# Kernel tuning notes

Measured on AMD Instinct MI355X. Metric: run time of the kernel, lower is better.

## Reference

```python
import jax, jax.numpy as jnp
import numpy as np

B, T, F, H = 8192, 96, 64, 256


def setup_inputs() -> dict:
    key = jax.random.key(0)
    ks = jax.random.split(key, 8)
    s = 0.05
    return {
        "decoder_feature": jax.random.normal(ks[0], (B, T, F), jnp.float32),
        "init_state": jax.random.normal(ks[1], (B, H), jnp.float32),
        "decoder_init_input": jax.random.normal(ks[2], (B, 1), jnp.float32),
        "kernel": jax.random.normal(ks[3], (1 + F, 3 * H), jnp.float32) * s,
        "recurrent_kernel": jax.random.normal(ks[4], (H, 3 * H), jnp.float32) * s,
        "input_bias": jnp.zeros((3 * H,), jnp.float32),
        "recurrent_bias": jnp.zeros((3 * H,), jnp.float32),
        "dense_w": jax.random.normal(ks[5], (H, 1), jnp.float32) * s,
        "dense_b": jnp.zeros((1,), jnp.float32),
        "predict_seq_length": T,
    }


def reference(decoder_feature, init_state, decoder_init_input, kernel,
              recurrent_kernel, input_bias, recurrent_bias, dense_w, dense_b,
              predict_seq_length):
    # teacher=None, use_attention=False path of Decoder2.forward.
    # Keras GRUCell (reset_after=True) recurrence, scanned over time.
    feats = jnp.swapaxes(decoder_feature[:, :predict_seq_length, :], 0, 1)  # [T,B,F]

    def step(carry, feat_t):
        prev_out, h = carry                                   # [B,1], [B,H]
        x = jnp.concatenate([prev_out, feat_t], axis=-1)      # [B,1+F]
        mx = x @ kernel + input_bias                          # [B,3H]
        mh = h @ recurrent_kernel + recurrent_bias            # [B,3H]
        xz, xr, xh = jnp.split(mx, 3, axis=-1)
        hz, hr, hh = jnp.split(mh, 3, axis=-1)
        z = jax.nn.sigmoid(xz + hz)
        r = jax.nn.sigmoid(xr + hr)
        cand = jnp.tanh(xh + r * hh)
        h_new = z * h + (1.0 - z) * cand
        out = h_new @ dense_w + dense_b                       # [B,1]
        return (out, h_new), out

    _, outs = jax.lax.scan(step, (decoder_init_input, init_state), feats)
    return jnp.swapaxes(outs, 0, 1)                           # [B,T,1]
```

## Files before the change

### kernel.cpp

```cpp
#include <hip/hip_runtime.h>


#define Bdim 8192
#define Tdim 96
#define Fdim 64
#define Hdim 256
#define BM   32
#define XS   72
#define HS   264
#define OS   97

typedef __attribute__((ext_vector_type(8))) short s16x8;
typedef __attribute__((ext_vector_type(4))) float f32x4;

#define MFMA __builtin_amdgcn_mfma_f32_16x16x32_bf16

__device__ __forceinline__ unsigned short f2bf(float f) {
    union { float f; unsigned u; } v; v.f = f;
    unsigned r = v.u + 0x7FFFu + ((v.u >> 16) & 1u);
    return (unsigned short)(r >> 16);
}

__global__ void prep_swz(const float* __restrict__ Wk, const float* __restrict__ Wr,
                         unsigned short* __restrict__ sW) {
    int idx = blockIdx.x * blockDim.x + threadIdx.x;
    if (idx >= 480 * 64) return;
    int lane = idx & 63, f = idx >> 6;
    int n2 = f & 1;
    int g  = (f >> 1) % 3;
    int kt = (f / 6) % 10;
    int w  = f / 60;
    int q = lane >> 4, cc = lane & 15;
    int n = g * 256 + w * 32 + n2 * 16 + cc;
    unsigned short* d = sW + (size_t)idx * 8;
#pragma unroll
    for (int j = 0; j < 8; ++j) {
        float v;
        if (kt < 8) v = Wr[(size_t)(kt * 32 + q * 8 + j) * 768 + n];
        else        v = Wk[(size_t)(1 + (kt - 8) * 32 + q * 8 + j) * 768 + n];
        d[j] = f2bf(v);
    }
}

__launch_bounds__(512, 1)
__global__ void gru_mfma6(
    const float* __restrict__ feat,
    const float* __restrict__ init_state,
    const float* __restrict__ init_inp,
    const unsigned short* __restrict__ sW,
    const float* __restrict__ Wk,
    const float* __restrict__ ib, const float* __restrict__ rb,
    const float* __restrict__ dw, const float* __restrict__ db,
    float* __restrict__ out)
{
    __shared__ __align__(16) unsigned short xs[BM * XS];
    __shared__ __align__(16) unsigned short hs[BM * HS];
    __shared__ float wpart[2][8][BM];
    __shared__ float outbuf[BM * OS];

    const int tid  = threadIdx.x;
    const int lane = tid & 63;
    const int w    = tid >> 6;
    const int q    = lane >> 4;
    const int c    = lane & 15;
    const int b0   = blockIdx.x * BM;

    float bz[2], brr[2], bxh[2], bhh[2], wk0z[2], wk0r[2], wk0h[2], dwv[2];
#pragma unroll
    for (int n2 = 0; n2 < 2; ++n2) {
        int col = w * 32 + n2 * 16 + c;
        bz[n2]   = ib[col]       + rb[col];
        brr[n2]  = ib[256 + col] + rb[256 + col];
        bxh[n2]  = ib[512 + col];
        bhh[n2]  = rb[512 + col];
        wk0z[n2] = Wk[col];
        wk0r[n2] = Wk[256 + col];
        wk0h[n2] = Wk[512 + col];
        dwv[n2]  = dw[col];
    }
    const float dbv = db[0];

    float hreg[2][2][4];
    float prevreg[2][4];
#pragma unroll
    for (int mt = 0; mt < 2; ++mt)
#pragma unroll
        for (int i = 0; i < 4; ++i) {
            int row = mt * 16 + q * 4 + i;
            prevreg[mt][i] = init_inp[b0 + row];
#pragma unroll
            for (int n2 = 0; n2 < 2; ++n2) {
                int col = w * 32 + n2 * 16 + c;
                float v = init_state[(size_t)(b0 + row) * Hdim + col];
                hreg[mt][n2][i] = v;
                hs[row * HS + col] = f2bf(v);
            }
        }

    {
        int r = tid >> 4, fi = tid & 15;
        float4 f = *(const float4*)&feat[((size_t)(b0 + r) * Tdim + 0) * Fdim + fi * 4];
        ushort4 p; p.x = f2bf(f.x); p.y = f2bf(f.y); p.z = f2bf(f.z); p.w = f2bf(f.w);
        *(ushort4*)&xs[r * XS + fi * 4] = p;
    }

    const unsigned short* wp0 = sW + (size_t)(w * 60) * 512 + lane * 8;

    __syncthreads();

    for (int t = 0; t < Tdim; ++t) {
        f32x4 az[2][2], arr[2][2], axh[2][2], ahh[2][2];
#pragma unroll
        for (int mt = 0; mt < 2; ++mt)
#pragma unroll
            for (int n2 = 0; n2 < 2; ++n2) {
                az[mt][n2] = (f32x4)0.0f; arr[mt][n2] = (f32x4)0.0f;
                axh[mt][n2] = (f32x4)0.0f; ahh[mt][n2] = (f32x4)0.0f;
            }

        s16x8 bf[3][6];
#pragma unroll
        for (int p = 0; p < 2; ++p) {
            const unsigned short* fp = wp0 + (size_t)(p * 6) * 512;
#pragma unroll
            for (int u = 0; u < 6; ++u) bf[p][u] = *(const s16x8*)(fp + u * 512);
        }

#pragma unroll
        for (int kt = 0; kt < 10; ++kt) {
            if (kt + 2 < 10) {
                const unsigned short* fp = wp0 + (size_t)((kt + 2) * 6) * 512;
#pragma unroll
                for (int u = 0; u < 6; ++u)
                    bf[(kt + 2) % 3][u] = *(const s16x8*)(fp + u * 512);
            }
            const s16x8* b = bf[kt % 3];
            s16x8 a0, a1;
            if (kt < 8) {
                a0 = *(const s16x8*)&hs[c * HS + kt * 32 + q * 8];
                a1 = *(const s16x8*)&hs[(16 + c) * HS + kt * 32 + q * 8];
            } else {
                a0 = *(const s16x8*)&xs[c * XS + (kt - 8) * 32 + q * 8];
                a1 = *(const s16x8*)&xs[(16 + c) * XS + (kt - 8) * 32 + q * 8];
            }
            az[0][0]  = MFMA(a0, b[0], az[0][0], 0, 0, 0);
            az[1][0]  = MFMA(a1, b[0], az[1][0], 0, 0, 0);
            az[0][1]  = MFMA(a0, b[1], az[0][1], 0, 0, 0);
            az[1][1]  = MFMA(a1, b[1], az[1][1], 0, 0, 0);
            arr[0][0] = MFMA(a0, b[2], arr[0][0], 0, 0, 0);
            arr[1][0] = MFMA(a1, b[2], arr[1][0], 0, 0, 0);
            arr[0][1] = MFMA(a0, b[3], arr[0][1], 0, 0, 0);
            arr[1][1] = MFMA(a1, b[3], arr[1][1], 0, 0, 0);
            if (kt < 8) {
                ahh[0][0] = MFMA(a0, b[4], ahh[0][0], 0, 0, 0);
                ahh[1][0] = MFMA(a1, b[4], ahh[1][0], 0, 0, 0);
                ahh[0][1] = MFMA(a0, b[5], ahh[0][1], 0, 0, 0);
                ahh[1][1] = MFMA(a1, b[5], ahh[1][1], 0, 0, 0);
            } else {
                axh[0][0] = MFMA(a0, b[4], axh[0][0], 0, 0, 0);
                axh[1][0] = MFMA(a1, b[4], axh[1][0], 0, 0, 0);
                axh[0][1] = MFMA(a0, b[5], axh[0][1], 0, 0, 0);
                axh[1][1] = MFMA(a1, b[5], axh[1][1], 0, 0, 0);
            }
        }
        __syncthreads();

        if (t > 0) {
            int r = lane & 31;
            float s = dbv;
            const float (*wp)[BM] = wpart[(t - 1) & 1];
#pragma unroll
            for (int ww = 0; ww < 8; ++ww) s += wp[ww][r];
            if (w == 0 && lane < 32) outbuf[r * OS + (t - 1)] = s;
#pragma unroll
            for (int mt = 0; mt < 2; ++mt)
#pragma unroll
                for (int i = 0; i < 4; ++i)
                    prevreg[mt][i] = __shfl(s, mt * 16 + q * 4 + i, 64);
        }

        float sd[2][4];
#pragma unroll
        for (int mt = 0; mt < 2; ++mt)
#pragma unroll
            for (int i = 0; i < 4; ++i) sd[mt][i] = 0.0f;

#pragma unroll
        for (int mt = 0; mt < 2; ++mt)
#pragma unroll
            for (int n2 = 0; n2 < 2; ++n2)
#pragma unroll
                for (int i = 0; i < 4; ++i) {
                    float pv = prevreg[mt][i];
                    float zz = 1.0f / (1.0f + __expf(-(az[mt][n2][i] + bz[n2] + pv * wk0z[n2])));
                    float rr = 1.0f / (1.0f + __expf(-(arr[mt][n2][i] + brr[n2] + pv * wk0r[n2])));
                    float cd = tanhf(axh[mt][n2][i] + bxh[n2] + pv * wk0h[n2] +
                                     rr * (ahh[mt][n2][i] + bhh[n2]));
                    float hn = zz * hreg[mt][n2][i] + (1.0f - zz) * cd;
                    hreg[mt][n2][i] = hn;
                    hs[(mt * 16 + q * 4 + i) * HS + w * 32 + n2 * 16 + c] = f2bf(hn);
                    sd[mt][i] += hn * dwv[n2];
                }

#pragma unroll
        for (int mt = 0; mt < 2; ++mt)
#pragma unroll
            for (int i = 0; i < 4; ++i) {
                float s = sd[mt][i];
                s += __shfl_xor(s, 1, 64);
                s += __shfl_xor(s, 2, 64);
                s += __shfl_xor(s, 4, 64);
                s += __shfl_xor(s, 8, 64);
                if (c == 0) wpart[t & 1][w][mt * 16 + q * 4 + i] = s;
            }

        if (t + 1 < Tdim) {
            int r = tid >> 4, fi = tid & 15;
            float4 f = *(const float4*)&feat[((size_t)(b0 + r) * Tdim + (t + 1)) * Fdim + fi * 4];
            ushort4 p; p.x = f2bf(f.x); p.y = f2bf(f.y); p.z = f2bf(f.z); p.w = f2bf(f.w);
            *(ushort4*)&xs[r * XS + fi * 4] = p;
        }
        __syncthreads();
    }

    {
        int r = lane & 31;
        float s = dbv;
        const float (*wp)[BM] = wpart[(Tdim - 1) & 1];
#pragma unroll
        for (int ww = 0; ww < 8; ++ww) s += wp[ww][r];
        if (w == 0 && lane < 32) outbuf[r * OS + (Tdim - 1)] = s;
    }
    __syncthreads();

    for (int i = tid; i < BM * Tdim; i += 512) {
        int r = i / Tdim, tt = i - r * Tdim;
        out[(size_t)b0 * Tdim + i] = outbuf[r * OS + tt];
    }
}

extern "C" void kernel_launch(void* const* d_in, const int* in_sizes, int n_in,
                              void* d_out, int out_size, void* d_ws, size_t ws_size,
                              hipStream_t stream) {
    const float* feat       = (const float*)d_in[0];
    const float* init_state = (const float*)d_in[1];
    const float* init_inp   = (const float*)d_in[2];
    const float* Wk         = (const float*)d_in[3];
    const float* Wr         = (const float*)d_in[4];
    const float* ib         = (const float*)d_in[5];
    const float* rb         = (const float*)d_in[6];
    const float* dw         = (const float*)d_in[7];
    const float* db         = (const float*)d_in[8];
    float* out              = (float*)d_out;

    unsigned short* sW = (unsigned short*)d_ws;

    prep_swz<<<120, 256, 0, stream>>>(Wk, Wr, sW);
    gru_mfma6<<<Bdim / BM, 512, 0, stream>>>(
        feat, init_state, init_inp, sW, Wk, ib, rb, dw, db, out);
}
```

Measured before the change: 1.723 ms.

## Split GRU step across 16 waves with double-buffered LDS and fast activations

Doubles the block to 1024 threads so each wave owns 16 hidden columns instead of 32, which halves per-wave MFMA and weight-register work. The h and x LDS tiles become double-buffered, so one of the two barriers per timestep can be dropped, and the next feature load is issued early. Sigmoid and tanh are replaced with exp plus hardware reciprocal approximations. The cost is more waves competing for the CU and weight-fetch traffic that rises with the wave count, plus a small loss of activation precision.

```diff
diff --git a/kernel.cpp b/kernel.cpp
--- a/kernel.cpp
+++ b/kernel.cpp
@@ -19,6 +19,13 @@
     union { float f; unsigned u; } v; v.f = f;
     unsigned r = v.u + 0x7FFFu + ((v.u >> 16) & 1u);
     return (unsigned short)(r >> 16);
+}
+
+__device__ __forceinline__ float sigm_fast(float x) {
+    return __builtin_amdgcn_rcpf(1.0f + __expf(-x));
+}
+__device__ __forceinline__ float tanh_fast(float x) {
+    return 1.0f - 2.0f * __builtin_amdgcn_rcpf(1.0f + __expf(2.0f * x));
 }
 
 __global__ void prep_swz(const float* __restrict__ Wk, const float* __restrict__ Wr,
@@ -42,8 +49,8 @@
     }
 }
 
-__launch_bounds__(512, 1)
-__global__ void gru_mfma6(
+__launch_bounds__(1024, 4)
+__global__ void gru_mfma8(
     const float* __restrict__ feat,
     const float* __restrict__ init_state,
     const float* __restrict__ init_inp,
@@ -53,34 +60,30 @@
     const float* __restrict__ dw, const float* __restrict__ db,
     float* __restrict__ out)
 {
-    __shared__ __align__(16) unsigned short xs[BM * XS];
-    __shared__ __align__(16) unsigned short hs[BM * HS];
-    __shared__ float wpart[2][8][BM];
+    __shared__ __align__(16) unsigned short xs[2][BM * XS];
+    __shared__ __align__(16) unsigned short hs[2][BM * HS];
+    __shared__ float wpart[2][16][BM];
     __shared__ float outbuf[BM * OS];
 
     const int tid  = threadIdx.x;
     const int lane = tid & 63;
-    const int w    = tid >> 6;
+    const int wv   = tid >> 6;
     const int q    = lane >> 4;
     const int c    = lane & 15;
     const int b0   = blockIdx.x * BM;
-
-    float bz[2], brr[2], bxh[2], bhh[2], wk0z[2], wk0r[2], wk0h[2], dwv[2];
-#pragma unroll
-    for (int n2 = 0; n2 < 2; ++n2) {
-        int col = w * 32 + n2 * 16 + c;
-        bz[n2]   = ib[col]       + rb[col];
-        brr[n2]  = ib[256 + col] + rb[256 + col];
-        bxh[n2]  = ib[512 + col];
-        bhh[n2]  = rb[512 + col];
-        wk0z[n2] = Wk[col];
-        wk0r[n2] = Wk[256 + col];
-        wk0h[n2] = Wk[512 + col];
-        dwv[n2]  = dw[col];
-    }
-    const float dbv = db[0];
-
-    float hreg[2][2][4];
+    const int col  = wv * 16 + c;
+
+    const float bz   = ib[col]       + rb[col];
+    const float brr  = ib[256 + col] + rb[256 + col];
+    const float bxh  = ib[512 + col];
+    const float bhh  = rb[512 + col];
+    const float wk0z = Wk[col];
+    const float wk0r = Wk[256 + col];
+    const float wk0h = Wk[512 + col];
+    const float dwv  = dw[col];
+    const float dbv  = db[0];
+
+    float hreg[2][4];
     float prevreg[2][4];
 #pragma unroll
     for (int mt = 0; mt < 2; ++mt)
@@ -88,90 +91,85 @@
         for (int i = 0; i < 4; ++i) {
             int row = mt * 16 + q * 4 + i;
             prevreg[mt][i] = init_inp[b0 + row];
-#pragma unroll
-            for (int n2 = 0; n2 < 2; ++n2) {
-                int col = w * 32 + n2 * 16 + c;
-                float v = init_state[(size_t)(b0 + row) * Hdim + col];
-                hreg[mt][n2][i] = v;
-                hs[row * HS + col] = f2bf(v);
-            }
+            float v = init_state[(size_t)(b0 + row) * Hdim + col];
+            hreg[mt][i] = v;
+            hs[0][row * HS + col] = f2bf(v);
         }
 
     {
-        int r = tid >> 4, fi = tid & 15;
-        float4 f = *(const float4*)&feat[((size_t)(b0 + r) * Tdim + 0) * Fdim + fi * 4];
-        ushort4 p; p.x = f2bf(f.x); p.y = f2bf(f.y); p.z = f2bf(f.z); p.w = f2bf(f.w);
-        *(ushort4*)&xs[r * XS + fi * 4] = p;
-    }
-
-    const unsigned short* wp0 = sW + (size_t)(w * 60) * 512 + lane * 8;
+        int r = tid >> 5, fi = tid & 31;
+        float2 f = *(const float2*)&feat[((size_t)(b0 + r) * Tdim + 0) * Fdim + fi * 2];
+        ushort2 p; p.x = f2bf(f.x); p.y = f2bf(f.y);
+        *(ushort2*)&xs[0][r * XS + fi * 2] = p;
+    }
+
+    const unsigned short* wp0 =
+        sW + ((size_t)(wv >> 1) * 60 + (wv & 1)) * 512 + lane * 8;
+
+    s16x8 bf[2][3];
+#pragma unroll
+    for (int g = 0; g < 3; ++g)
+        bf[0][g] = *(const s16x8*)(wp0 + (size_t)g * 1024);
 
     __syncthreads();
 
     for (int t = 0; t < Tdim; ++t) {
-        f32x4 az[2][2], arr[2][2], axh[2][2], ahh[2][2];
-#pragma unroll
-        for (int mt = 0; mt < 2; ++mt)
-#pragma unroll
-            for (int n2 = 0; n2 < 2; ++n2) {
-                az[mt][n2] = (f32x4)0.0f; arr[mt][n2] = (f32x4)0.0f;
-                axh[mt][n2] = (f32x4)0.0f; ahh[mt][n2] = (f32x4)0.0f;
-            }
-
-        s16x8 bf[3][6];
-#pragma unroll
-        for (int p = 0; p < 2; ++p) {
-            const unsigned short* fp = wp0 + (size_t)(p * 6) * 512;
-#pragma unroll
-            for (int u = 0; u < 6; ++u) bf[p][u] = *(const s16x8*)(fp + u * 512);
+        const unsigned short* hsp = hs[t & 1];
+        const unsigned short* xsp = xs[t & 1];
+
+        f32x4 az[2], ar[2], ax[2], ah[2];
+#pragma unroll
+        for (int mt = 0; mt < 2; ++mt) {
+            az[mt] = (f32x4)0.0f; ar[mt] = (f32x4)0.0f;
+            ax[mt] = (f32x4)0.0f; ah[mt] = (f32x4)0.0f;
         }
 
 #pragma unroll
         for (int kt = 0; kt < 10; ++kt) {
-            if (kt + 2 < 10) {
-                const unsigned short* fp = wp0 + (size_t)((kt + 2) * 6) * 512;
-#pragma unroll
-                for (int u = 0; u < 6; ++u)
-                    bf[(kt + 2) % 3][u] = *(const s16x8*)(fp + u * 512);
-            }
-            const s16x8* b = bf[kt % 3];
+            if (kt + 1 < 10) {
+#pragma unroll
+                for (int g = 0; g < 3; ++g)
+                    bf[(kt + 1) & 1][g] =
+                        *(const s16x8*)(wp0 + (size_t)((kt + 1) * 3 + g) * 1024);
+            }
+            const s16x8* b = bf[kt & 1];
             s16x8 a0, a1;
             if (kt < 8) {
-                a0 = *(const s16x8*)&hs[c * HS + kt * 32 + q * 8];
-                a1 = *(const s16x8*)&hs[(16 + c) * HS + kt * 32 + q * 8];
+                a0 = *(const s16x8*)&hsp[c * HS + kt * 32 + q * 8];
+                a1 = *(const s16x8*)&hsp[(16 + c) * HS + kt * 32 + q * 8];
             } else {
-                a0 = *(const s16x8*)&xs[c * XS + (kt - 8) * 32 + q * 8];
-                a1 = *(const s16x8*)&xs[(16 + c) * XS + (kt - 8) * 32 + q * 8];
-            }
-            az[0][0]  = MFMA(a0, b[0], az[0][0], 0, 0, 0);
-            az[1][0]  = MFMA(a1, b[0], az[1][0], 0, 0, 0);
-            az[0][1]  = MFMA(a0, b[1], az[0][1], 0, 0, 0);
-            az[1][1]  = MFMA(a1, b[1], az[1][1], 0, 0, 0);
-            arr[0][0] = MFMA(a0, b[2], arr[0][0], 0, 0, 0);
-            arr[1][0] = MFMA(a1, b[2], arr[1][0], 0, 0, 0);
-            arr[0][1] = MFMA(a0, b[3], arr[0][1], 0, 0, 0);
-            arr[1][1] = MFMA(a1, b[3], arr[1][1], 0, 0, 0);
+                a0 = *(const s16x8*)&xsp[c * XS + (kt - 8) * 32 + q * 8];
+                a1 = *(const s16x8*)&xsp[(16 + c) * XS + (kt - 8) * 32 + q * 8];
+            }
+            az[0] = MFMA(a0, b[0], az[0], 0, 0, 0);
+            az[1] = MFMA(a1, b[0], az[1], 0, 0, 0);
+            ar[0] = MFMA(a0, b[1], ar[0], 0, 0, 0);
+            ar[1] = MFMA(a1, b[1], ar[1], 0, 0, 0);
             if (kt < 8) {
-                ahh[0][0] = MFMA(a0, b[4], ahh[0][0], 0, 0, 0);
-                ahh[1][0] = MFMA(a1, b[4], ahh[1][0], 0, 0, 0);
-                ahh[0][1] = MFMA(a0, b[5], ahh[0][1], 0, 0, 0);
-                ahh[1][1] = MFMA(a1, b[5], ahh[1][1], 0, 0, 0);
+                ah[0] = MFMA(a0, b[2], ah[0], 0, 0, 0);
+                ah[1] = MFMA(a1, b[2], ah[1], 0, 0, 0);
             } else {
-                axh[0][0] = MFMA(a0, b[4], axh[0][0], 0, 0, 0);
-                axh[1][0] = MFMA(a1, b[4], axh[1][0], 0, 0, 0);
-                axh[0][1] = MFMA(a0, b[5], axh[0][1], 0, 0, 0);
-                axh[1][1] = MFMA(a1, b[5], axh[1][1], 0, 0, 0);
-            }
-        }
-        __syncthreads();
+                ax[0] = MFMA(a0, b[2], ax[0], 0, 0, 0);
+                ax[1] = MFMA(a1, b[2], ax[1], 0, 0, 0);
+            }
+        }
+
+#pragma unroll
+        for (int g = 0; g < 3; ++g)
+            bf[0][g] = *(const s16x8*)(wp0 + (size_t)g * 1024);
+
+        float2 fnext;
+        int fr = tid >> 5, ffi = tid & 31;
+        if (t + 1 < Tdim)
+            fnext = *(const float2*)&feat[((size_t)(b0 + fr) * Tdim + (t + 1)) * Fdim + ffi * 2];
 
         if (t > 0) {
             int r = lane & 31;
             float s = dbv;
             const float (*wp)[BM] = wpart[(t - 1) & 1];
 #pragma unroll
-            for (int ww = 0; ww < 8; ++ww) s += wp[ww][r];
-            if (w == 0 && lane < 32) outbuf[r * OS + (t - 1)] = s;
+            for (int ww = 0; ww < 16; ++ww) s += wp[ww][r];
+            if (wv == 0 && lane < 32) outbuf[r * OS + (t - 1)] = s;
 #pragma unroll
             for (int mt = 0; mt < 2; ++mt)
 #pragma unroll
@@ -179,46 +177,30 @@
                     prevreg[mt][i] = __shfl(s, mt * 16 + q * 4 + i, 64);
         }
 
-        float sd[2][4];
+        unsigned short* hsn = hs[(t + 1) & 1];
 #pragma unroll
         for (int mt = 0; mt < 2; ++mt)
 #pragma unroll
-            for (int i = 0; i < 4; ++i) sd[mt][i] = 0.0f;
-
-#pragma unroll
-        for (int mt = 0; mt < 2; ++mt)
-#pragma unroll
-            for (int n2 = 0; n2 < 2; ++n2)
-#pragma unroll
-                for (int i = 0; i < 4; ++i) {
-                    float pv = prevreg[mt][i];
-                    float zz = 1.0f / (1.0f + __expf(-(az[mt][n2][i] + bz[n2] + pv * wk0z[n2])));
-                    float rr = 1.0f / (1.0f + __expf(-(arr[mt][n2][i] + brr[n2] + pv * wk0r[n2])));
-                    float cd = tanhf(axh[mt][n2][i] + bxh[n2] + pv * wk0h[n2] +
-                                     rr * (ahh[mt][n2][i] + bhh[n2]));
-                    float hn = zz * hreg[mt][n2][i] + (1.0f - zz) * cd;
-                    hreg[mt][n2][i] = hn;
-                    hs[(mt * 16 + q * 4 + i) * HS + w * 32 + n2 * 16 + c] = f2bf(hn);
-                    sd[mt][i] += hn * dwv[n2];
-                }
-
-#pragma unroll
-        for (int mt = 0; mt < 2; ++mt)
-#pragma unroll
             for (int i = 0; i < 4; ++i) {
-                float s = sd[mt][i];
+                float pv = prevreg[mt][i];
+                float zz = sigm_fast(az[mt][i] + bz + pv * wk0z);
+                float rr = sigm_fast(ar[mt][i] + brr + pv * wk0r);
+                float cd = tanh_fast(ax[mt][i] + bxh + pv * wk0h +
+                                     rr * (ah[mt][i] + bhh));
+                float hn = zz * hreg[mt][i] + (1.0f - zz) * cd;
+                hreg[mt][i] = hn;
+                hsn[(mt * 16 + q * 4 + i) * HS + col] = f2bf(hn);
+                float s = hn * dwv;
                 s += __shfl_xor(s, 1, 64);
                 s += __shfl_xor(s, 2, 64);
                 s += __shfl_xor(s, 4, 64);
                 s += __shfl_xor(s, 8, 64);
-                if (c == 0) wpart[t & 1][w][mt * 16 + q * 4 + i] = s;
+                if (c == 0) wpart[t & 1][wv][mt * 16 + q * 4 + i] = s;
             }
 
         if (t + 1 < Tdim) {
-            int r = tid >> 4, fi = tid & 15;
-            float4 f = *(const float4*)&feat[((size_t)(b0 + r) * Tdim + (t + 1)) * Fdim + fi * 4];
-            ushort4 p; p.x = f2bf(f.x); p.y = f2bf(f.y); p.z = f2bf(f.z); p.w = f2bf(f.w);
-            *(ushort4*)&xs[r * XS + fi * 4] = p;
+            ushort2 p; p.x = f2bf(fnext.x); p.y = f2bf(fnext.y);
+            *(ushort2*)&xs[(t + 1) & 1][fr * XS + ffi * 2] = p;
         }
         __syncthreads();
     }
@@ -228,12 +210,12 @@
         float s = dbv;
         const float (*wp)[BM] = wpart[(Tdim - 1) & 1];
 #pragma unroll
-        for (int ww = 0; ww < 8; ++ww) s += wp[ww][r];
-        if (w == 0 && lane < 32) outbuf[r * OS + (Tdim - 1)] = s;
+        for (int ww = 0; ww < 16; ++ww) s += wp[ww][r];
+        if (wv == 0 && lane < 32) outbuf[r * OS + (Tdim - 1)] = s;
     }
     __syncthreads();
 
-    for (int i = tid; i < BM * Tdim; i += 512) {
+    for (int i = tid; i < BM * Tdim; i += 1024) {
         int r = i / Tdim, tt = i - r * Tdim;
         out[(size_t)b0 * Tdim + i] = outbuf[r * OS + tt];
     }
@@ -256,6 +238,6 @@
     unsigned short* sW = (unsigned short*)d_ws;
 
     prep_swz<<<120, 256, 0, stream>>>(Wk, Wr, sW);
-    gru_mfma6<<<Bdim / BM, 512, 0, stream>>>(
+    gru_mfma8<<<Bdim / BM, 1024, 0, stream>>>(
         feat, init_state, init_inp, sW, Wk, ib, rb, dw, db, out);
 }
```

Result: faster. 1.645 ms (-4.5%).
